# Performance work log

Measured on AMD Instinct MI355X. Metric: run time of the kernel, lower is better.

## Reference

```python
import jax, jax.numpy as jnp
import numpy as np

B, N, D_IN, D_OUT, NUM_RING = 32, 8192, 64, 128, 4
BN_EPS = 1e-5


def setup_inputs() -> dict:
    key = jax.random.key(0)
    ks = jax.random.split(key, 8)
    return {
        "x": jax.random.normal(ks[0], (B, D_IN, N), dtype=jnp.float32),
        "ring": jax.random.randint(ks[1], (B, N), 0, NUM_RING, dtype=jnp.int64),
        "W": jax.random.normal(ks[2], (NUM_RING, D_OUT, D_IN), dtype=jnp.float32) * 0.1,
        "b": jax.random.normal(ks[3], (NUM_RING, D_OUT), dtype=jnp.float32) * 0.1,
        "gamma": jax.random.uniform(ks[4], (NUM_RING, D_OUT), dtype=jnp.float32) + 0.5,
        "beta": jax.random.normal(ks[5], (NUM_RING, D_OUT), dtype=jnp.float32) * 0.1,
        "mean": jax.random.normal(ks[6], (NUM_RING, D_OUT), dtype=jnp.float32) * 0.1,
        "var": jax.random.uniform(ks[7], (NUM_RING, D_OUT), dtype=jnp.float32) + 0.5,
    }


def reference(x, ring, W, b, gamma, beta, mean, var):
    # x: [B, 64, N]; ring: [B, N] int labels in [0, num_ring)
    xt = jnp.transpose(x, (0, 2, 1))  # [B, N, 64]
    Bv, Nv, _ = xt.shape
    num_ring = W.shape[0]
    out = jnp.zeros((Bv, Nv, W.shape[1]), dtype=x.dtype)
    neg = jnp.finfo(x.dtype).min
    for i in range(num_ring):  # small fixed loop over rings
        # 1x1 conv == per-point linear, then BatchNorm (inference-mode affine)
        y = jnp.einsum("bnd,od->bno", xt, W[i]) + b[i]  # [B, N, 128]
        scale = gamma[i] * jax.lax.rsqrt(var[i] + BN_EPS)
        y = (y - mean[i]) * scale + beta[i]
        m = (ring == i)[..., None]  # [B, N, 1]
        # per-(batch, ring) segment max over points, broadcast back to members
        ymax = jnp.max(jnp.where(m, y, neg), axis=1, keepdims=True)  # [B, 1, 128]
        out = jnp.where(m, ymax, out)
    return jnp.transpose(out, (0, 2, 1))  # [B, 128, N]
```

## Files before the change

kernel.cpp:

```cpp
#include <hip/hip_runtime.h>
#include <hip/hip_bf16.h>
#include <cstdint>
#include <cstddef>

#define BB 32
#define NN 8192
#define DIN 64
#define DOUT 128
#define NR 4
#define BN_EPS 1e-5f
#define CHUNKS 8

typedef float nfloat4 __attribute__((ext_vector_type(4)));
typedef float floatx4 __attribute__((ext_vector_type(4)));
typedef short short8 __attribute__((ext_vector_type(8)));


__device__ inline void pack2(float a, float b, short8& dst, int idx) {
  __hip_bfloat162 h = __float22bfloat162_rn(make_float2(a, b));
  const unsigned int bits = *(unsigned int*)&h;
  dst[idx] = (short)(bits & 0xffffu);
  dst[idx + 1] = (short)(bits >> 16);
}

__device__ inline int swz(int n) { return (n ^ (n >> 2) ^ (n >> 5)) & 7; }

__global__ void __launch_bounds__(512) k_compute(
    const float* __restrict__ x, const float* __restrict__ W,
    const int* __restrict__ ring, float* __restrict__ part) {
  const int b = blockIdx.y;
  const int big = blockIdx.x;
  const int n0 = big * 1024;
  const int tid = (int)threadIdx.x;
  const int wave = tid >> 6;
  const int lane = tid & 63;
  const int quad = lane >> 4;
  const int l16 = lane & 15;
  const float* xb = x + (size_t)b * DIN * NN;
  const int* rgb = ring + (size_t)b * NN + n0;

  __shared__ short8 lx[2][256 * 8];

  short8 afr[NR][2];
#pragma unroll
  for (int r = 0; r < NR; ++r) {
    const int chan = wave * 16 + l16;
    const float* wr = W + ((size_t)r * DOUT + chan) * DIN + quad * 8;
#pragma unroll
    for (int ks = 0; ks < 2; ++ks) {
      const float4 w0 = *(const float4*)&wr[ks * 32];
      const float4 w1 = *(const float4*)&wr[ks * 32 + 4];
      short8 a;
      pack2(w0.x, w0.y, a, 0);
      pack2(w0.z, w0.w, a, 2);
      pack2(w1.x, w1.y, a, 4);
      pack2(w1.z, w1.w, a, 6);
      afr[r][ks] = a;
    }
  }

  floatx4 rmax[NR];
#pragma unroll
  for (int r = 0; r < NR; ++r)
    rmax[r] = {-INFINITY, -INFINITY, -INFINITY, -INFINITY};

  auto LOADL = [&](nfloat4 (&L)[8], int c) {
    const float* base = xb + (size_t)(wave * 8) * NN + n0 + c * 256 + 4 * lane;
#pragma unroll
    for (int j = 0; j < 8; ++j)
      L[j] = *(const nfloat4*)&base[(size_t)j * NN];
  };
  auto PACKW = [&](int buf, const nfloat4 (&L)[8]) {
#pragma unroll
    for (int i = 0; i < 4; ++i) {
      short8 v;
      pack2(L[0][i], L[1][i], v, 0);
      pack2(L[2][i], L[3][i], v, 2);
      pack2(L[4][i], L[5][i], v, 4);
      pack2(L[6][i], L[7][i], v, 6);
      const int ni = 4 * lane + i;
      lx[buf][ni * 8 + (wave ^ swz(ni))] = v;
    }
  };
  auto TLOOP = [&](int buf, int c) {
#pragma unroll 4
    for (int T = 0; T < 16; ++T) {
      const int n = T * 16 + l16;
      const short8 b0 = lx[buf][n * 8 + (quad ^ swz(n))];
      const short8 b1 = lx[buf][n * 8 + ((4 + quad) ^ swz(n))];
      const int rr = rgb[c * 256 + n];
#pragma unroll
      for (int r = 0; r < NR; ++r) {
        floatx4 acc = {0.f, 0.f, 0.f, 0.f};
        acc = __builtin_amdgcn_mfma_f32_16x16x32_bf16(afr[r][0], b0, acc, 0, 0, 0);
        acc = __builtin_amdgcn_mfma_f32_16x16x32_bf16(afr[r][1], b1, acc, 0, 0, 0);
        if (rr == r) {
#pragma unroll
          for (int p = 0; p < 4; ++p) rmax[r][p] = fmaxf(rmax[r][p], acc[p]);
        }
      }
    }
  };

  nfloat4 LA[8], LB[8];
  LOADL(LA, 0);
  PACKW(0, LA);
  LOADL(LB, 1);
  __syncthreads();
  TLOOP(0, 0);
  PACKW(1, LB);
  LOADL(LA, 2);
  __syncthreads();
  TLOOP(1, 1);
  PACKW(0, LA);
  LOADL(LB, 3);
  __syncthreads();
  TLOOP(0, 2);
  PACKW(1, LB);
  __syncthreads();
  TLOOP(1, 3);

  float* slot = part + (size_t)(b * CHUNKS + big) * NR * DOUT;
#pragma unroll
  for (int r = 0; r < NR; ++r) {
#pragma unroll
    for (int p = 0; p < 4; ++p) {
      float v = rmax[r][p];
      v = fmaxf(v, __shfl_xor(v, 1, 64));
      v = fmaxf(v, __shfl_xor(v, 2, 64));
      v = fmaxf(v, __shfl_xor(v, 4, 64));
      v = fmaxf(v, __shfl_xor(v, 8, 64));
      if (l16 == 0) {
        const int chan = wave * 16 + quad * 4 + p;
        slot[r * DOUT + chan] = v;
      }
    }
  }
}

__global__ void __launch_bounds__(256) k_out(
    const float* __restrict__ bias, const float* __restrict__ gamma,
    const float* __restrict__ beta, const float* __restrict__ mean,
    const float* __restrict__ var, const int* __restrict__ ring,
    const float* __restrict__ part, float* __restrict__ out) {
  const int b = blockIdx.z;
  const int og = blockIdx.y;
  const int n0 = blockIdx.x * 1024;
  const int t = (int)threadIdx.x;

  __shared__ float lut[32 * NR * 32];
  {
    const int oo = t >> 3;
    const int r = (t >> 1) & 3;
    const int c0 = (t & 1) * 16;
    const int o = og * 32 + oo;
    const float* ps = part + (size_t)b * CHUNKS * NR * DOUT + r * DOUT + o;
    float raw = -INFINITY;
#pragma unroll
    for (int c = 0; c < CHUNKS; ++c)
      raw = fmaxf(raw, ps[(size_t)c * NR * DOUT]);
    const int tt = r * DOUT + o;
    const float sc = gamma[tt] * rsqrtf(var[tt] + BN_EPS);
    const float val = (raw + bias[tt] - mean[tt]) * sc + beta[tt];
    nfloat4 v4 = {val, val, val, val};
    float* dst = &lut[(oo * NR + r) * 32 + c0];
#pragma unroll
    for (int k = 0; k < 4; ++k) *(nfloat4*)&dst[k * 4] = v4;
  }
  __syncthreads();

  const int n = n0 + t * 4;
  const int4 rg = *(const int4*)&ring[(size_t)b * NN + n];
  const int l31 = t & 31;
  const float* p0 = &lut[rg.x * 32 + l31];
  const float* p1 = &lut[rg.y * 32 + l31];
  const float* p2 = &lut[rg.z * 32 + l31];
  const float* p3 = &lut[rg.w * 32 + l31];
  float* orow = out + ((size_t)b * DOUT + og * 32) * NN + n;

#pragma unroll 8
  for (int oo = 0; oo < 32; ++oo) {
    nfloat4 v;
    v.x = p0[oo * 128];
    v.y = p1[oo * 128];
    v.z = p2[oo * 128];
    v.w = p3[oo * 128];
    *(nfloat4*)(orow + (size_t)oo * NN) = v;
  }
}

extern "C" void kernel_launch(void* const* d_in, const int* in_sizes, int n_in,
                              void* d_out, int out_size, void* d_ws, size_t ws_size,
                              hipStream_t stream) {
  const float* x = (const float*)d_in[0];
  const int* ring = (const int*)d_in[1];
  const float* W = (const float*)d_in[2];
  const float* bias = (const float*)d_in[3];
  const float* gamma = (const float*)d_in[4];
  const float* beta = (const float*)d_in[5];
  const float* mean = (const float*)d_in[6];
  const float* var = (const float*)d_in[7];
  float* out = (float*)d_out;

  float* part = (float*)d_ws;

  k_compute<<<dim3(NN / 1024, BB), 512, 0, stream>>>(x, W, ring, part);
  k_out<<<dim3(NN / 1024, DOUT / 32, BB), 256, 0, stream>>>(bias, gamma, beta, mean,
                                                            var, ring, part, out);
}
```

Before: 225.9 us.

## Remap blocks to XCDs by batch and replace LDS lookup with register selects

Both kernels now use a flat 1D grid whose block index is decoded so that each XCD handles a contiguous set of batches, keeping ring and partial data local to one XCD's L2. The output kernel drops the shared-memory lookup table and barrier. Each block now covers two output channels across all 8192 points, and the four per-ring values are picked from registers with selects. This cuts LDS traffic and sync, at the cost of reading the ring labels once per channel pair and doing less work per block on the write side.

```diff
diff --git a/kernel.cpp b/kernel.cpp
--- a/kernel.cpp
+++ b/kernel.cpp
@@ -28,8 +28,11 @@
 __global__ void __launch_bounds__(512) k_compute(
     const float* __restrict__ x, const float* __restrict__ W,
     const int* __restrict__ ring, float* __restrict__ part) {
-  const int b = blockIdx.y;
-  const int big = blockIdx.x;
+  const int g = (int)blockIdx.x;
+  const int xcd = g & 7;
+  const int idx = g >> 3;
+  const int b = 4 * xcd + (idx >> 3);
+  const int big = idx & 7;
   const int n0 = big * 1024;
   const int tid = (int)threadIdx.x;
   const int wave = tid >> 6;
@@ -143,49 +146,66 @@
     const float* __restrict__ beta, const float* __restrict__ mean,
     const float* __restrict__ var, const int* __restrict__ ring,
     const float* __restrict__ part, float* __restrict__ out) {
-  const int b = blockIdx.z;
-  const int og = blockIdx.y;
-  const int n0 = blockIdx.x * 1024;
+  const int g = (int)blockIdx.x;
+  const int xcd = g & 7;
+  const int idx = g >> 3;
+  const int b = 4 * xcd + (idx >> 6);
+  const int o0 = (idx & 63) * 2;
   const int t = (int)threadIdx.x;
 
-  __shared__ float lut[32 * NR * 32];
+  float ya0, ya1, ya2, ya3, yb0, yb1, yb2, yb3;
   {
-    const int oo = t >> 3;
-    const int r = (t >> 1) & 3;
-    const int c0 = (t & 1) * 16;
-    const int o = og * 32 + oo;
-    const float* ps = part + (size_t)b * CHUNKS * NR * DOUT + r * DOUT + o;
-    float raw = -INFINITY;
-#pragma unroll
-    for (int c = 0; c < CHUNKS; ++c)
-      raw = fmaxf(raw, ps[(size_t)c * NR * DOUT]);
-    const int tt = r * DOUT + o;
-    const float sc = gamma[tt] * rsqrtf(var[tt] + BN_EPS);
-    const float val = (raw + bias[tt] - mean[tt]) * sc + beta[tt];
-    nfloat4 v4 = {val, val, val, val};
-    float* dst = &lut[(oo * NR + r) * 32 + c0];
-#pragma unroll
-    for (int k = 0; k < 4; ++k) *(nfloat4*)&dst[k * 4] = v4;
-  }
-  __syncthreads();
-
-  const int n = n0 + t * 4;
-  const int4 rg = *(const int4*)&ring[(size_t)b * NN + n];
-  const int l31 = t & 31;
-  const float* p0 = &lut[rg.x * 32 + l31];
-  const float* p1 = &lut[rg.y * 32 + l31];
-  const float* p2 = &lut[rg.z * 32 + l31];
-  const float* p3 = &lut[rg.w * 32 + l31];
-  float* orow = out + ((size_t)b * DOUT + og * 32) * NN + n;
-
-#pragma unroll 8
-  for (int oo = 0; oo < 32; ++oo) {
-    nfloat4 v;
-    v.x = p0[oo * 128];
-    v.y = p1[oo * 128];
-    v.z = p2[oo * 128];
-    v.w = p3[oo * 128];
-    *(nfloat4*)(orow + (size_t)oo * NN) = v;
+    float tmp[2][NR];
+#pragma unroll
+    for (int oo = 0; oo < 2; ++oo) {
+#pragma unroll
+      for (int r = 0; r < NR; ++r) {
+        const int o = o0 + oo;
+        const float* ps = part + (size_t)b * CHUNKS * NR * DOUT + r * DOUT + o;
+        float raw = -INFINITY;
+#pragma unroll
+        for (int c = 0; c < CHUNKS; ++c)
+          raw = fmaxf(raw, ps[(size_t)c * NR * DOUT]);
+        const int tt = r * DOUT + o;
+        const float sc = gamma[tt] * rsqrtf(var[tt] + BN_EPS);
+        tmp[oo][r] = (raw + bias[tt] - mean[tt]) * sc + beta[tt];
+      }
+    }
+    ya0 = tmp[0][0]; ya1 = tmp[0][1]; ya2 = tmp[0][2]; ya3 = tmp[0][3];
+    yb0 = tmp[1][0]; yb1 = tmp[1][1]; yb2 = tmp[1][2]; yb3 = tmp[1][3];
+  }
+
+  const int* rgb = ring + (size_t)b * NN;
+  float* r0 = out + ((size_t)b * DOUT + o0) * NN;
+  float* r1 = r0 + NN;
+
+  int4 rg[8];
+#pragma unroll
+  for (int it = 0; it < 8; ++it)
+    rg[it] = *(const int4*)&rgb[it * 1024 + t * 4];
+
+#pragma unroll
+  for (int it = 0; it < 8; ++it) {
+    const int n = it * 1024 + t * 4;
+    nfloat4 va, vb;
+    { const int r = rg[it].x;
+      const float la = (r & 1) ? ya1 : ya0, ha = (r & 1) ? ya3 : ya2;
+      const float lb = (r & 1) ? yb1 : yb0, hb = (r & 1) ? yb3 : yb2;
+      va.x = (r & 2) ? ha : la; vb.x = (r & 2) ? hb : lb; }
+    { const int r = rg[it].y;
+      const float la = (r & 1) ? ya1 : ya0, ha = (r & 1) ? ya3 : ya2;
+      const float lb = (r & 1) ? yb1 : yb0, hb = (r & 1) ? yb3 : yb2;
+      va.y = (r & 2) ? ha : la; vb.y = (r & 2) ? hb : lb; }
+    { const int r = rg[it].z;
+      const float la = (r & 1) ? ya1 : ya0, ha = (r & 1) ? ya3 : ya2;
+      const float lb = (r & 1) ? yb1 : yb0, hb = (r & 1) ? yb3 : yb2;
+      va.z = (r & 2) ? ha : la; vb.z = (r & 2) ? hb : lb; }
+    { const int r = rg[it].w;
+      const float la = (r & 1) ? ya1 : ya0, ha = (r & 1) ? ya3 : ya2;
+      const float lb = (r & 1) ? yb1 : yb0, hb = (r & 1) ? yb3 : yb2;
+      va.w = (r & 2) ? ha : la; vb.w = (r & 2) ? hb : lb; }
+    *(nfloat4*)&r0[n] = va;
+    *(nfloat4*)&r1[n] = vb;
   }
 }
 
@@ -204,7 +224,7 @@
 
   float* part = (float*)d_ws;
 
-  k_compute<<<dim3(NN / 1024, BB), 512, 0, stream>>>(x, W, ring, part);
-  k_out<<<dim3(NN / 1024, DOUT / 32, BB), 256, 0, stream>>>(bias, gamma, beta, mean,
-                                                            var, ring, part, out);
-}
+  k_compute<<<dim3(256), 512, 0, stream>>>(x, W, ring, part);
+  k_out<<<dim3(2048), 256, 0, stream>>>(bias, gamma, beta, mean,
+                                        var, ring, part, out);
+}
```

Measured after the change: 229.5 us. About the same (+1.6%).

## Halve compute-block span to double grid and reduce partial maxima through LDS

Applied to the files above, without the earlier changes.

Each k_compute block now covers 512 points instead of 1024, so the grid has twice as many blocks (16 chunks per batch) and each block runs only two pipelined tiles. The shuffle-based max reduction is replaced by staging per-lane maxima in shared memory (reusing the tile buffer) and reducing with vector loads. Launch bounds now request 4 blocks per CU. The aim is higher occupancy and better latency hiding across the GPU, at the cost of more partial results for k_out to merge and an extra LDS round-trip with syncs.

```diff
diff --git a/kernel.cpp b/kernel.cpp
--- a/kernel.cpp
+++ b/kernel.cpp
@@ -9,7 +9,7 @@
 #define DOUT 128
 #define NR 4
 #define BN_EPS 1e-5f
-#define CHUNKS 8
+#define CHUNKS 16
 
 typedef float nfloat4 __attribute__((ext_vector_type(4)));
 typedef float floatx4 __attribute__((ext_vector_type(4)));
@@ -25,12 +25,12 @@
 
 __device__ inline int swz(int n) { return (n ^ (n >> 2) ^ (n >> 5)) & 7; }
 
-__global__ void __launch_bounds__(512) k_compute(
+__global__ void __launch_bounds__(512, 4) k_compute(
     const float* __restrict__ x, const float* __restrict__ W,
     const int* __restrict__ ring, float* __restrict__ part) {
   const int b = blockIdx.y;
-  const int big = blockIdx.x;
-  const int n0 = big * 1024;
+  const int chunk = blockIdx.x;
+  const int n0 = chunk * 512;
   const int tid = (int)threadIdx.x;
   const int wave = tid >> 6;
   const int lane = tid & 63;
@@ -109,32 +109,35 @@
   __syncthreads();
   TLOOP(0, 0);
   PACKW(1, LB);
-  LOADL(LA, 2);
   __syncthreads();
   TLOOP(1, 1);
-  PACKW(0, LA);
-  LOADL(LB, 3);
-  __syncthreads();
-  TLOOP(0, 2);
-  PACKW(1, LB);
-  __syncthreads();
-  TLOOP(1, 3);
-
-  float* slot = part + (size_t)(b * CHUNKS + big) * NR * DOUT;
-#pragma unroll
-  for (int r = 0; r < NR; ++r) {
-#pragma unroll
-    for (int p = 0; p < 4; ++p) {
-      float v = rmax[r][p];
-      v = fmaxf(v, __shfl_xor(v, 1, 64));
-      v = fmaxf(v, __shfl_xor(v, 2, 64));
-      v = fmaxf(v, __shfl_xor(v, 4, 64));
-      v = fmaxf(v, __shfl_xor(v, 8, 64));
-      if (l16 == 0) {
-        const int chan = wave * 16 + quad * 4 + p;
-        slot[r * DOUT + chan] = v;
-      }
-    }
+
+  __syncthreads();
+  float* red = (float*)&lx[0][0];
+#pragma unroll
+  for (int r = 0; r < NR; ++r)
+#pragma unroll
+    for (int p = 0; p < 4; ++p)
+      red[(r * 4 + p) * 520 + tid] = rmax[r][p];
+  __syncthreads();
+
+  {
+    const int l = tid & 63;
+    const int w = tid >> 6;
+    const int r = l >> 4;
+    const int p = (l >> 2) & 3;
+    const int q = l & 3;
+    const float* src = &red[(r * 4 + p) * 520 + w * 64 + q * 16];
+    nfloat4 a = *(const nfloat4*)&src[0];
+    nfloat4 c = *(const nfloat4*)&src[4];
+    nfloat4 d = *(const nfloat4*)&src[8];
+    nfloat4 e = *(const nfloat4*)&src[12];
+    float v = fmaxf(fmaxf(fmaxf(a.x, a.y), fmaxf(a.z, a.w)),
+                    fmaxf(fmaxf(c.x, c.y), fmaxf(c.z, c.w)));
+    v = fmaxf(v, fmaxf(fmaxf(d.x, d.y), fmaxf(d.z, d.w)));
+    v = fmaxf(v, fmaxf(fmaxf(e.x, e.y), fmaxf(e.z, e.w)));
+    float* slot = part + (size_t)(b * CHUNKS + chunk) * NR * DOUT;
+    slot[r * DOUT + w * 16 + q * 4 + p] = v;
   }
 }
 
@@ -204,7 +207,7 @@
 
   float* part = (float*)d_ws;
 
-  k_compute<<<dim3(NN / 1024, BB), 512, 0, stream>>>(x, W, ring, part);
+  k_compute<<<dim3(CHUNKS, BB), 512, 0, stream>>>(x, W, ring, part);
   k_out<<<dim3(NN / 1024, DOUT / 32, BB), 256, 0, stream>>>(bias, gamma, beta, mean,
                                                             var, ring, part, out);
 }
```

New measurement: 220.1 us. 2.6% less time.
